# Optimization experiments

Measured on AMD Instinct MI355X. Metric: run time of the kernel, lower is better.

## Reference

```python
import jax, jax.numpy as jnp
import numpy as np

LENS = 0.4
DECAY = 0.2
THRESH = 0.2
LOG_SIG_MIN, LOG_SIG_MAX = -20.0, 2.0

# Surrogate-gradient spike: forward is heaviside, backward is rectangular window |x|<lens
@jax.custom_vjp
def act_fun(x):
    return (x > 0.0).astype(x.dtype)

def _act_fwd(x):
    return act_fun(x), x

def _act_bwd(x, g):
    return (g * (jnp.abs(x) < LENS).astype(g.dtype),)

act_fun.defvjp(_act_fwd, _act_bwd)


def _xavier(k, shape):
    fan_out, fan_in = shape
    lim = float(np.sqrt(6.0 / (fan_in + fan_out)))
    return jax.random.uniform(k, shape, jnp.float32, -lim, lim)


def setup_inputs() -> dict:
    key = jax.random.key(0)
    ks = jax.random.split(key, 9)
    B, IN, H, A = 4096, 512, 2048, 32
    return {
        "state": jax.random.normal(ks[0], (B, 5, IN), jnp.float32),
        "W_lif": _xavier(ks[1], (H, IN)), "b_lif": jnp.zeros((H,), jnp.float32),
        "W11": _xavier(ks[2], (H, H)), "b11": jnp.zeros((H,), jnp.float32),
        "W12": _xavier(ks[3], (H, H)), "b12": jnp.zeros((H,), jnp.float32),
        "W21": _xavier(ks[4], (H, H)), "b21": jnp.zeros((H,), jnp.float32),
        "W22": _xavier(ks[5], (H, H)), "b22": jnp.zeros((H,), jnp.float32),
        "Wm": _xavier(ks[6], (A, H)), "bm": jnp.zeros((A,), jnp.float32),
        "Wls": _xavier(ks[7], (A, H)), "bls": jnp.zeros((A,), jnp.float32),
    }


def reference(state, W_lif, b_lif, W11, b11, W12, b12, W21, b21, W22, b22, Wm, bm, Wls, bls):
    x_seq = jnp.repeat(state, 3, axis=1)
    # precompute fc(x) for all steps in one GEMM: [B,15,H]
    fc = jnp.einsum('bti,hi->bth', x_seq, W_lif) + b_lif
    B, T, H = fc.shape

    def step(carry, fc_t):
        mem, spike = carry
        mem1 = mem * DECAY * (1.0 - spike) + fc_t
        spike1 = act_fun(mem1 - THRESH)
        return (mem1, spike1), spike1

    init = (jnp.zeros((B, H), fc.dtype), jnp.zeros((B, H), fc.dtype))
    _, spikes = jax.lax.scan(step, init, jnp.swapaxes(fc, 0, 1))  # [T,B,H]
    x = jnp.mean(spikes, axis=0)  # [B,H]

    x1 = jax.nn.relu(x @ W11.T + b11)
    x1 = jax.nn.relu(x1 @ W12.T + b12)
    mean = x1 @ Wm.T + bm

    x2 = jax.nn.relu(x @ W21.T + b21)
    x2 = jax.nn.relu(x2 @ W22.T + b22)
    log_std = jnp.clip(x2 @ Wls.T + bls, LOG_SIG_MIN, LOG_SIG_MAX)
    return mean, log_std
```

## Files before the change

kernel.cpp:

```cpp
#include <hip/hip_runtime.h>
#include <hip/hip_bf16.h>


typedef _Float16 f16;
using f32x4 = __attribute__((ext_vector_type(4))) float;
using f16x8 = __attribute__((ext_vector_type(8))) f16;

#define MFMA16(a, b, c) __builtin_amdgcn_mfma_f32_16x16x32_f16((a), (b), (c), 0, 0, 0)
#define VMW8()  asm volatile("s_waitcnt vmcnt(8)" ::: "memory")
#define VMW4()  asm volatile("s_waitcnt vmcnt(4)" ::: "memory")
#define VMW0()  asm volatile("s_waitcnt vmcnt(0)" ::: "memory")
#define LGKM0() asm volatile("s_waitcnt lgkmcnt(0)" ::: "memory")
#define BARRIER() __builtin_amdgcn_s_barrier()
#define SCHED0() __builtin_amdgcn_sched_barrier(0)

__device__ __forceinline__ void gload16(const void* g, void* l) {
  __builtin_amdgcn_global_load_lds(
      (const __attribute__((address_space(1))) unsigned int*)g,
      (__attribute__((address_space(3))) unsigned int*)l, 16, 0, 0);
}

__device__ __forceinline__ void cvt8(const float4& a, const float4& b, f16* dst) {
  f16x8 d;
  d[0] = (f16)a.x; d[1] = (f16)a.y; d[2] = (f16)a.z; d[3] = (f16)a.w;
  d[4] = (f16)b.x; d[5] = (f16)b.y; d[6] = (f16)b.z; d[7] = (f16)b.w;
  *(f16x8*)dst = d;
}

__global__ __launch_bounds__(256) void cvt2b_kernel(
    const float* __restrict__ s0, f16* __restrict__ d0, int n8a,
    const float* __restrict__ s1, f16* __restrict__ d1, int n8b)
{
  int i = blockIdx.x * 256 + threadIdx.x;
  const float* src; f16* dst; int k;
  if (i < n8a) { src = s0; dst = d0; k = i; }
  else { k = i - n8a; if (k >= n8b) return; src = s1; dst = d1; }
  const float4* s4 = (const float4*)src;
  float4 a = s4[(size_t)k * 2], b = s4[(size_t)k * 2 + 1];
  cvt8(a, b, dst + (size_t)k * 8);
}

__global__ __launch_bounds__(256) void cvt4_kernel(
    const float* __restrict__ w0, const float* __restrict__ w1,
    const float* __restrict__ w2, const float* __restrict__ w3,
    f16* __restrict__ dst)
{
  int i = blockIdx.x * 256 + threadIdx.x;
  int which = i >> 19, k = i & 524287;
  const float* src = (which == 0) ? w0 : (which == 1) ? w1 : (which == 2) ? w2 : w3;
  const float4* s4 = (const float4*)src;
  float4 a = s4[(size_t)k * 2], b = s4[(size_t)k * 2 + 1];
  cvt8(a, b, dst + (size_t)i * 8);
}

__global__ __launch_bounds__(256) void cvt2_kernel(
    const float* __restrict__ s0, const float* __restrict__ s1,
    f16* __restrict__ d0, f16* __restrict__ d1, int n8each)
{
  int i = blockIdx.x * 256 + threadIdx.x;
  const float* src = (i < n8each) ? s0 : s1;
  f16* dst = (i < n8each) ? d0 : d1;
  int k = (i < n8each) ? i : i - n8each;
  if (k >= n8each) return;
  const float4* s4 = (const float4*)src;
  float4 a = s4[(size_t)k * 2], b = s4[(size_t)k * 2 + 1];
  cvt8(a, b, dst + (size_t)k * 8);
}

__global__ __launch_bounds__(512, 1) void lif256_kernel(
    const f16* __restrict__ S,
    const f16* __restrict__ W,
    const float* __restrict__ bl,
    f16* __restrict__ X)
{
  __shared__ alignas(16) f16 lds[6][128 * 64];

  const int tid = threadIdx.x, wid = tid >> 6, lane = tid & 63;
  const int wg = ((int)blockIdx.x % 8) * 64 + (int)blockIdx.x / 8;
  const int bn = wg & 15, bm = wg >> 4;
  const int b0 = bm * 128, h0 = bn * 128;
  const int wr0 = (wid >> 2) * 64, wc0 = (wid & 3) * 32;
  const int fr = lane & 15, fq = lane >> 4;
  const int sr = tid >> 3, scb = (tid & 7) * 16;

  f32x4 acc[4][2] = {};
  float mem[4][2][4] = {};
  float cnt[4][2][4] = {};

  char* Lb = (char*)&lds[0][0];
  const int xsw = (fr & 7) << 4;
  const int x0 = (fq * 16) ^ xsw;
  const int x1 = (64 + fq * 16) ^ xsw;
  char* const pA0 = Lb + (wr0 + fr) * 128 + x0;
  char* const pA1 = Lb + (wr0 + fr) * 128 + x1;
  char* const pB0 = Lb + 49152 + (wc0 + fr) * 128 + x0;
  char* const pB1 = Lb + 49152 + (wc0 + fr) * 128 + x1;

  const f16* sBase[2]; const f16* wBase[2];
#pragma unroll
  for (int l = 0; l < 2; ++l) {
    const int row = l * 64 + sr;
    const int c2 = scb ^ ((row & 7) << 4);
    sBase[l] = S + (size_t)(b0 + row) * 2560 + (c2 >> 1);
    wBase[l] = W + (size_t)(h0 + row) * 512 + (c2 >> 1);
  }

  auto STAGE = [&](int soSt, int g) {
    const int koff = (g >> 3) * 512 + (g & 7) * 64;
    const int kw = (g & 7) * 64;
#pragma unroll
    for (int l = 0; l < 2; ++l)
      gload16(sBase[l] + koff, Lb + soSt + l * 8192 + tid * 16);
#pragma unroll
    for (int l = 0; l < 2; ++l)
      gload16(wBase[l] + kw, Lb + 49152 + soSt + l * 8192 + tid * 16);
  };

  const float bias[2] = { bl[h0 + wc0 + fr], bl[h0 + wc0 + 16 + fr] };

  STAGE(0, 0);
  STAGE(16384, 1);
  VMW4();
  BARRIER();
  SCHED0();

  int soRead = 0, soStage = 32768;
  for (int g = 0; g < 40; ++g) {
    if (g + 2 < 40) STAGE(soStage, g + 2);
    SCHED0();

    f16x8 b[2][2], a0[2][2], a1[2][2];
#pragma unroll
    for (int nf = 0; nf < 2; ++nf) {
      b[nf][0] = *(const f16x8*)(pB0 + soRead + nf * 2048);
      b[nf][1] = *(const f16x8*)(pB1 + soRead + nf * 2048);
    }
#pragma unroll
    for (int i = 0; i < 2; ++i) {
      a0[i][0] = *(const f16x8*)(pA0 + soRead + i * 2048);
      a0[i][1] = *(const f16x8*)(pA1 + soRead + i * 2048);
      a1[i][0] = *(const f16x8*)(pA0 + soRead + (2 + i) * 2048);
      a1[i][1] = *(const f16x8*)(pA1 + soRead + (2 + i) * 2048);
    }

    __builtin_amdgcn_s_setprio(1);
#pragma unroll
    for (int i = 0; i < 2; ++i)
#pragma unroll
      for (int nf = 0; nf < 2; ++nf) {
        acc[i][nf] = MFMA16(a0[i][0], b[nf][0], acc[i][nf]);
        acc[i][nf] = MFMA16(a0[i][1], b[nf][1], acc[i][nf]);
      }
#pragma unroll
    for (int i = 0; i < 2; ++i)
#pragma unroll
      for (int nf = 0; nf < 2; ++nf) {
        acc[2 + i][nf] = MFMA16(a1[i][0], b[nf][0], acc[2 + i][nf]);
        acc[2 + i][nf] = MFMA16(a1[i][1], b[nf][1], acc[2 + i][nf]);
      }
    __builtin_amdgcn_s_setprio(0);

    if ((g & 7) == 7) {
#pragma unroll
      for (int mf = 0; mf < 4; ++mf)
#pragma unroll
        for (int nf = 0; nf < 2; ++nf) {
#pragma unroll
          for (int r = 0; r < 4; ++r) {
            const float fc = acc[mf][nf][r] + bias[nf];
            float m = mem[mf][nf][r], c = cnt[mf][nf][r];
#pragma unroll
            for (int j = 0; j < 3; ++j) {
              m = ((m > 0.2f) ? 0.f : m * 0.2f) + fc;
              c += (m > 0.2f) ? 1.f : 0.f;
            }
            mem[mf][nf][r] = m; cnt[mf][nf][r] = c;
          }
          acc[mf][nf] = f32x4{0.f, 0.f, 0.f, 0.f};
        }
    }

    LGKM0();
    if (g + 2 < 40)      { VMW4(); }
    else if (g + 1 < 40) { VMW0(); }
    BARRIER();
    SCHED0();

    soRead  = (soRead  == 32768) ? 0 : soRead  + 16384;
    soStage = (soStage == 32768) ? 0 : soStage + 16384;
  }

#pragma unroll
  for (int nf = 0; nf < 2; ++nf) {
    const int col = h0 + wc0 + nf * 16 + fr;
#pragma unroll
    for (int mf = 0; mf < 4; ++mf) {
      const int row0 = b0 + wr0 + mf * 16 + fq * 4;
#pragma unroll
      for (int r = 0; r < 4; ++r)
        X[(size_t)(row0 + r) * 2048 + col] = (f16)(cnt[mf][nf][r] / 15.0f);
    }
  }
}

__global__ __launch_bounds__(512, 2) void trunk256_kernel(
    const f16* __restrict__ A0, const f16* __restrict__ A1, int lda,
    const f16* __restrict__ W0, const f16* __restrict__ W1,
    const float* __restrict__ bb0, const float* __restrict__ bb1,
    f16* __restrict__ C0, f16* __restrict__ C1, int ldc,
    int nbm, int nbn_half, int K)
{
  __shared__ alignas(16) f16 lds[4][256 * 64];

  const int tid = threadIdx.x, wid = tid >> 6, lane = tid & 63;
  const int nwg = nbm * nbn_half * 2, q8 = nwg / 8;
  const int wg = ((int)blockIdx.x % 8) * q8 + (int)blockIdx.x / 8;
  const int bmi = wg % nbm, t = wg / nbm;
  const int half = (t >= nbn_half);
  const f16* Ap = half ? A1 : A0;
  const f16* Wp = half ? W1 : W0;
  const float* bias = half ? bb1 : bb0;
  f16* C = half ? C1 : C0;
  const int bm0 = bmi * 256;
  const int bn0 = (half ? t - nbn_half : t) * 256;

  const int wr0 = (wid >> 2) * 128, wc0 = (wid & 3) * 64;
  const int fr = lane & 15, fq = lane >> 4;
  const int sr = tid >> 3, scb = (tid & 7) * 16;

  f32x4 acc[8][4] = {};
  const int NT = K / 64;

  char* Lb = (char*)&lds[0][0];
  const int xsw = (fr & 7) << 4;
  const int x0 = (fq * 16) ^ xsw;
  const int x1 = (64 + fq * 16) ^ xsw;
  char* const pA0 = Lb + (wr0 + fr) * 128 + x0;
  char* const pA1 = Lb + (wr0 + fr) * 128 + x1;
  char* const pB0 = Lb + 65536 + (wc0 + fr) * 128 + x0;
  char* const pB1 = Lb + 65536 + (wc0 + fr) * 128 + x1;

  const f16* aBase[4]; const f16* wBase[4];
#pragma unroll
  for (int l = 0; l < 4; ++l) {
    const int row = l * 64 + sr;
    const int c2 = scb ^ ((row & 7) << 4);
    aBase[l] = Ap + (size_t)(bm0 + row) * lda + (c2 >> 1);
    wBase[l] = Wp + (size_t)(bn0 + row) * K + (c2 >> 1);
  }

  auto STAGE = [&](int slot, int kt) {
    const int koff = kt * 64;
#pragma unroll
    for (int l = 0; l < 4; ++l)
      gload16(aBase[l] + koff, Lb + slot * 32768 + l * 8192 + tid * 16);
#pragma unroll
    for (int l = 0; l < 4; ++l)
      gload16(wBase[l] + koff, Lb + 65536 + slot * 32768 + l * 8192 + tid * 16);
  };

  STAGE(0, 0);
  STAGE(1, 1);
  VMW8();
  BARRIER();
  SCHED0();

#pragma unroll 2
  for (int kt = 0; kt < NT; ++kt) {
    const int slot = kt & 1;
    const int so = slot * 32768;

    f16x8 b[4][2];
#pragma unroll
    for (int nf = 0; nf < 4; ++nf) {
      b[nf][0] = *(const f16x8*)(pB0 + so + nf * 2048);
      b[nf][1] = *(const f16x8*)(pB1 + so + nf * 2048);
    }
    f16x8 a0[2][2], a1[2][2];
#pragma unroll
    for (int i = 0; i < 2; ++i) {
      a0[i][0] = *(const f16x8*)(pA0 + so + i * 2048);
      a0[i][1] = *(const f16x8*)(pA1 + so + i * 2048);
    }

    auto QUAD = [&](int mbase, f16x8 (&a)[2][2]) {
      __builtin_amdgcn_s_setprio(1);
#pragma unroll
      for (int nf = 0; nf < 4; ++nf) {
        acc[mbase][nf]     = MFMA16(a[0][0], b[nf][0], acc[mbase][nf]);
        acc[mbase][nf]     = MFMA16(a[0][1], b[nf][1], acc[mbase][nf]);
        acc[mbase + 1][nf] = MFMA16(a[1][0], b[nf][0], acc[mbase + 1][nf]);
        acc[mbase + 1][nf] = MFMA16(a[1][1], b[nf][1], acc[mbase + 1][nf]);
      }
      __builtin_amdgcn_s_setprio(0);
    };

#pragma unroll
    for (int i = 0; i < 2; ++i) {
      a1[i][0] = *(const f16x8*)(pA0 + so + (2 + i) * 2048);
      a1[i][1] = *(const f16x8*)(pA1 + so + (2 + i) * 2048);
    }
    QUAD(0, a0);
#pragma unroll
    for (int i = 0; i < 2; ++i) {
      a0[i][0] = *(const f16x8*)(pA0 + so + (4 + i) * 2048);
      a0[i][1] = *(const f16x8*)(pA1 + so + (4 + i) * 2048);
    }
    QUAD(2, a1);
#pragma unroll
    for (int i = 0; i < 2; ++i) {
      a1[i][0] = *(const f16x8*)(pA0 + so + (6 + i) * 2048);
      a1[i][1] = *(const f16x8*)(pA1 + so + (6 + i) * 2048);
    }
    QUAD(4, a0);
    QUAD(6, a1);

    LGKM0();
    BARRIER();
    SCHED0();
    if (kt + 2 < NT) {
      STAGE(slot, kt + 2);
      SCHED0();
      VMW8();
    } else if (kt + 1 < NT) {
      VMW0();
    }
    BARRIER();
    SCHED0();
  }

#pragma unroll
  for (int nf = 0; nf < 4; ++nf) {
    const int col = bn0 + wc0 + nf * 16 + fr;
    const float bv = bias[col];
#pragma unroll
    for (int m = 0; m < 8; ++m) {
      const int row0 = bm0 + wr0 + m * 16 + fq * 4;
#pragma unroll
      for (int r = 0; r < 4; ++r) {
        float v = fmaxf(acc[m][nf][r] + bv, 0.f);
        C[(size_t)(row0 + r) * ldc + col] = (f16)v;
      }
    }
  }
}

__global__ __launch_bounds__(256) void head_kernel(
    const f16* __restrict__ H1, const f16* __restrict__ H2,
    const f16* __restrict__ Wm, const float* __restrict__ bm,
    const f16* __restrict__ Wls, const float* __restrict__ bls,
    float* __restrict__ OUT, int M, int K)
{
  const int tid = threadIdx.x, wid = tid >> 6, lane = tid & 63;
  const int m0 = blockIdx.x * 64 + wid * 16;
  const int kb = (lane >> 4) * 8, fr = lane & 15, fq = lane >> 4;

  f32x4 a1[2] = {}, a2[2] = {};
  for (int k0 = 0; k0 < K; k0 += 32) {
    f16x8 f1 = *(const f16x8*)&H1[(size_t)(m0 + fr) * K + k0 + kb];
    f16x8 f2 = *(const f16x8*)&H2[(size_t)(m0 + fr) * K + k0 + kb];
#pragma unroll
    for (int n = 0; n < 2; ++n) {
      f16x8 wm = *(const f16x8*)&Wm[(size_t)(n * 16 + fr) * K + k0 + kb];
      f16x8 wl = *(const f16x8*)&Wls[(size_t)(n * 16 + fr) * K + k0 + kb];
      a1[n] = MFMA16(f1, wm, a1[n]);
      a2[n] = MFMA16(f2, wl, a2[n]);
    }
  }

#pragma unroll
  for (int n = 0; n < 2; ++n) {
    const int col = n * 16 + fr;
    const float bvm = bm[col];
    const float bvl = bls[col];
#pragma unroll
    for (int r = 0; r < 4; ++r) {
      const int row = m0 + fq * 4 + r;
      OUT[(size_t)row * 32 + col] = a1[n][r] + bvm;
      float lv = a2[n][r] + bvl;
      OUT[(size_t)M * 32 + (size_t)row * 32 + col] = fminf(fmaxf(lv, -20.f), 2.f);
    }
  }
}

extern "C" void kernel_launch(void* const* d_in, const int* in_sizes, int n_in,
                              void* d_out, int out_size, void* d_ws, size_t ws_size,
                              hipStream_t stream) {
  const float* state = (const float*)d_in[0];
  const float* W_lif = (const float*)d_in[1];
  const float* b_lif = (const float*)d_in[2];
  const float* W11   = (const float*)d_in[3];
  const float* b11   = (const float*)d_in[4];
  const float* W12   = (const float*)d_in[5];
  const float* b12   = (const float*)d_in[6];
  const float* W21   = (const float*)d_in[7];
  const float* b21   = (const float*)d_in[8];
  const float* W22   = (const float*)d_in[9];
  const float* b22   = (const float*)d_in[10];
  const float* Wm    = (const float*)d_in[11];
  const float* bm    = (const float*)d_in[12];
  const float* Wls   = (const float*)d_in[13];
  const float* bls   = (const float*)d_in[14];
  float* out = (float*)d_out;

  const int B = 4096, IN = 512, H = 2048;
  char* ws = (char*)d_ws;
  f16* x    = (f16*)(ws);
  f16* h1   = (f16*)(ws + 16777216);
  f16* h2   = (f16*)(ws + 33554432);
  f16* s16  = (f16*)(ws + 50331648);
  f16* wl16 = (f16*)(ws + 71303168);
  f16* w4   = (f16*)(ws + 50331648);
  f16* w11h = (f16*)(ws + 50331648);
  f16* w21h = (f16*)(ws + 58720256);
  f16* w12h = (f16*)(ws + 67108864);
  f16* w22h = (f16*)(ws + 75497472);
  f16* h22  = (f16*)(ws + 50331648);
  f16* wmh  = (f16*)(ws + 67108864);
  f16* wlsh = (f16*)(ws + 67239936);
  f16* h12  = x;

  const int n8s = B * 5 * IN / 8, n8w = H * IN / 8;
  cvt2b_kernel<<<(n8s + n8w + 255) / 256, 256, 0, stream>>>(
      state, s16, n8s, W_lif, wl16, n8w);

  lif256_kernel<<<512, 512, 0, stream>>>(s16, wl16, b_lif, x);

  cvt4_kernel<<<4 * 524288 / 256, 256, 0, stream>>>(W11, W21, W12, W22, w4);

  trunk256_kernel<<<256, 512, 0, stream>>>(x, x, H, w11h, w21h, b11, b21,
                                           h1, h2, H, 16, 8, H);
  trunk256_kernel<<<256, 512, 0, stream>>>(h1, h2, H, w12h, w22h, b12, b22,
                                           h12, h22, H, 16, 8, H);

  cvt2_kernel<<<2 * (32 * H / 8) / 256, 256, 0, stream>>>(Wm, Wls, wmh, wlsh, 32 * H / 8);
  head_kernel<<<B / 64, 256, 0, stream>>>(h12, h22, wmh, bm, wlsh, bls, out, B, H);
}
```

Baseline: 269.2 us.

## Split A/B tile prefetch and issue loads earlier within the k-loop

The single end-of-iteration stage of A and W tiles is split into separate A and B stages. The W tile for k+2 is issued right after the B fragments are read into registers, and the A tile is issued before the last MFMA quad, so global-to-LDS loads overlap more of the MFMA work. This adds two extra barriers and more lgkmcnt waits per iteration, which may stall waves. The vmcnt accounting still has to match the new issue order.

```diff
diff --git a/kernel.cpp b/kernel.cpp
--- a/kernel.cpp
+++ b/kernel.cpp
@@ -249,18 +249,21 @@
     wBase[l] = Wp + (size_t)(bn0 + row) * K + (c2 >> 1);
   }
 
-  auto STAGE = [&](int slot, int kt) {
+  auto STAGE_A = [&](int slot, int kt) {
     const int koff = kt * 64;
 #pragma unroll
     for (int l = 0; l < 4; ++l)
       gload16(aBase[l] + koff, Lb + slot * 32768 + l * 8192 + tid * 16);
+  };
+  auto STAGE_B = [&](int slot, int kt) {
+    const int koff = kt * 64;
 #pragma unroll
     for (int l = 0; l < 4; ++l)
       gload16(wBase[l] + koff, Lb + 65536 + slot * 32768 + l * 8192 + tid * 16);
   };
 
-  STAGE(0, 0);
-  STAGE(1, 1);
+  STAGE_A(0, 0); STAGE_B(0, 0);
+  STAGE_A(1, 1); STAGE_B(1, 1);
   VMW8();
   BARRIER();
   SCHED0();
@@ -270,20 +273,7 @@
     const int slot = kt & 1;
     const int so = slot * 32768;
 
-    f16x8 b[4][2];
-#pragma unroll
-    for (int nf = 0; nf < 4; ++nf) {
-      b[nf][0] = *(const f16x8*)(pB0 + so + nf * 2048);
-      b[nf][1] = *(const f16x8*)(pB1 + so + nf * 2048);
-    }
-    f16x8 a0[2][2], a1[2][2];
-#pragma unroll
-    for (int i = 0; i < 2; ++i) {
-      a0[i][0] = *(const f16x8*)(pA0 + so + i * 2048);
-      a0[i][1] = *(const f16x8*)(pA1 + so + i * 2048);
-    }
-
-    auto QUAD = [&](int mbase, f16x8 (&a)[2][2]) {
+    auto QUAD = [&](int mbase, f16x8 (&b)[4][2], f16x8 (&a)[2][2]) {
       __builtin_amdgcn_s_setprio(1);
 #pragma unroll
       for (int nf = 0; nf < 4; ++nf) {
@@ -295,36 +285,49 @@
       __builtin_amdgcn_s_setprio(0);
     };
 
+    f16x8 b[4][2], a0[2][2], a1[2][2];
+#pragma unroll
+    for (int nf = 0; nf < 4; ++nf) {
+      b[nf][0] = *(const f16x8*)(pB0 + so + nf * 2048);
+      b[nf][1] = *(const f16x8*)(pB1 + so + nf * 2048);
+    }
+#pragma unroll
+    for (int i = 0; i < 2; ++i) {
+      a0[i][0] = *(const f16x8*)(pA0 + so + i * 2048);
+      a0[i][1] = *(const f16x8*)(pA1 + so + i * 2048);
+    }
+    LGKM0();
+    BARRIER();
+    if (kt + 2 < NT) STAGE_B(slot, kt + 2);
+    SCHED0();
+
 #pragma unroll
     for (int i = 0; i < 2; ++i) {
       a1[i][0] = *(const f16x8*)(pA0 + so + (2 + i) * 2048);
       a1[i][1] = *(const f16x8*)(pA1 + so + (2 + i) * 2048);
     }
-    QUAD(0, a0);
+    QUAD(0, b, a0);
+    LGKM0(); SCHED0();
 #pragma unroll
     for (int i = 0; i < 2; ++i) {
       a0[i][0] = *(const f16x8*)(pA0 + so + (4 + i) * 2048);
       a0[i][1] = *(const f16x8*)(pA1 + so + (4 + i) * 2048);
     }
-    QUAD(2, a1);
+    QUAD(2, b, a1);
+    LGKM0(); SCHED0();
 #pragma unroll
     for (int i = 0; i < 2; ++i) {
       a1[i][0] = *(const f16x8*)(pA0 + so + (6 + i) * 2048);
       a1[i][1] = *(const f16x8*)(pA1 + so + (6 + i) * 2048);
     }
-    QUAD(4, a0);
-    QUAD(6, a1);
-
+    QUAD(4, b, a0);
     LGKM0();
     BARRIER();
+    if (kt + 2 < NT) STAGE_A(slot, kt + 2);
     SCHED0();
-    if (kt + 2 < NT) {
-      STAGE(slot, kt + 2);
-      SCHED0();
-      VMW8();
-    } else if (kt + 1 < NT) {
-      VMW0();
-    }
+    QUAD(6, b, a1);
+    if (kt + 2 < NT)      { VMW8(); }
+    else if (kt + 1 < NT) { VMW0(); }
     BARRIER();
     SCHED0();
   }
```

New measurement: 265.0 us. Within noise of the previous version (-1.6%).
